# Optimization experiments

Hardware: AMD Instinct MI355X
Metric: run time of the kernel (lower is better)

The kernel has to match this reference:

```python
import jax, jax.numpy as jnp
import numpy as np
from jax import lax

B, S, H, T = 64, 512, 768, 9


def setup_inputs() -> dict:
    key = jax.random.key(0)
    ks = jax.random.split(key, 7)
    hidden = jax.random.normal(ks[0], (B, S, H), dtype=jnp.float32)
    W = jax.random.normal(ks[1], (H, T), dtype=jnp.float32) * 0.02
    b = jax.random.normal(ks[2], (T,), dtype=jnp.float32) * 0.02
    start_trans = jax.random.normal(ks[3], (T,), dtype=jnp.float32) * 0.1
    end_trans = jax.random.normal(ks[4], (T,), dtype=jnp.float32) * 0.1
    trans = jax.random.normal(ks[5], (T, T), dtype=jnp.float32) * 0.1
    labels = jax.random.randint(ks[6], (B, S), 0, T, dtype=jnp.int64)
    return {"hidden": hidden, "W": W, "b": b, "start_trans": start_trans,
            "end_trans": end_trans, "trans": trans, "labels": labels}


def _crf_nll(emissions, labels, start_trans, end_trans, trans):
    # emissions: [B,S,T], labels: [B,S] int. mask = labels > -1 (torchcrf semantics).
    maskf = (labels > -1).astype(emissions.dtype)          # [B,S]
    tags = jnp.maximum(labels, 0)                          # safe indexing

    # ---- numerator: score of the gold path ----
    tags0 = tags[:, 0]                                     # [B]
    num0 = start_trans[tags0] + jnp.take_along_axis(emissions[:, 0], tags0[:, None], axis=1)[:, 0]

    em_t = jnp.swapaxes(emissions[:, 1:], 0, 1)            # [S-1,B,T]
    tg_t = jnp.swapaxes(tags[:, 1:], 0, 1)                 # [S-1,B]
    mk_t = jnp.swapaxes(maskf[:, 1:], 0, 1)                # [S-1,B]

    def num_step(carry, xs):
        score, prev = carry
        em, tg, mk = xs
        step = trans[prev, tg] + jnp.take_along_axis(em, tg[:, None], axis=1)[:, 0]
        score = score + step * mk
        prev = jnp.where(mk > 0, tg, prev)
        return (score, prev), None

    (num, last_tags), _ = lax.scan(num_step, (num0, tags0), (em_t, tg_t, mk_t))
    num = num + end_trans[last_tags]                       # [B]

    # ---- denominator: log-partition via forward algorithm (log-semiring scan) ----
    alpha0 = start_trans[None, :] + emissions[:, 0]        # [B,T]

    def den_step(alpha, xs):
        em, mk = xs
        new = jax.nn.logsumexp(alpha[:, :, None] + trans[None, :, :], axis=1) + em  # [B,T]
        alpha = jnp.where(mk[:, None] > 0, new, alpha)
        return alpha, None

    alpha, _ = lax.scan(den_step, alpha0, (em_t, mk_t))
    den = jax.nn.logsumexp(alpha + end_trans[None, :], axis=1)  # [B]

    # model returns -crf(...) with reduction='mean'  =>  mean NLL
    return jnp.mean(den - num)


def reference(hidden, W, b, start_trans, end_trans, trans, labels):
    # token-classification head: [B,S,H] @ [H,T] -> emissions [B,S,T]
    emissions = jnp.einsum('bsh,ht->bst', hidden, W) + b
    return _crf_nll(emissions, labels, start_trans, end_trans, trans)
```

## Files before the change

### kernel.cpp

```cpp
#include <hip/hip_runtime.h>

constexpr int Bn = 64, Sn = 512, Hn = 768, Tn = 9;
constexpr int EMS = 12;
constexpr int CHUNKS = 32, CLEN = 16;
constexpr int WPAD = 776;

__device__ __forceinline__ float lse9(const float* e) {
    float m01 = fmaxf(e[0], e[1]), m23 = fmaxf(e[2], e[3]);
    float m45 = fmaxf(e[4], e[5]), m67 = fmaxf(e[6], e[7]);
    float m = fmaxf(fmaxf(fmaxf(m01, m23), fmaxf(m45, m67)), e[8]);
    float s = 0.f;
#pragma unroll
    for (int k = 0; k < 9; ++k) s += __expf(e[k] - m);
    return m + __logf(s);
}

__global__ __launch_bounds__(256, 1) void emis_kernel(
        const float* __restrict__ hidden, const float* __restrict__ W,
        const float* __restrict__ bias, float* __restrict__ em) {
    __shared__ float Wt[Tn * WPAD];
    const int tid = threadIdx.x;
    const int lane = tid & 63;

    for (int f = tid; f < Hn * Tn; f += 256) {
        int h = f / 9, t = f - 9 * h;
        Wt[t * WPAD + h] = W[f];
    }
    const float myb = (lane < 9) ? bias[lane] : 0.f;
    __syncthreads();

    float4 wq[27];
#pragma unroll
    for (int t = 0; t < 9; ++t)
#pragma unroll
        for (int k = 0; k < 3; ++k)
            wq[t * 3 + k] = *reinterpret_cast<const float4*>(
                &Wt[t * WPAD + 4 * lane + 256 * k]);

    const int wid = blockIdx.x * 4 + (tid >> 6);
    const int nw  = gridDim.x * 4;
    const int nrows = Bn * Sn;

    int row = wid;
    const float4* hp = reinterpret_cast<const float4*>(hidden + (size_t)row * Hn);
    float4 p0 = hp[lane], p1 = hp[lane + 64], p2 = hp[lane + 128];

    for (; row < nrows; ) {
        const int nxt = row + nw;
        float4 c0 = p0, c1 = p1, c2 = p2;
        if (nxt < nrows) {
            const float4* hq = reinterpret_cast<const float4*>(hidden + (size_t)nxt * Hn);
            p0 = hq[lane]; p1 = hq[lane + 64]; p2 = hq[lane + 128];
        }
        const float hv[12] = {c0.x, c0.y, c0.z, c0.w, c1.x, c1.y, c1.z, c1.w,
                              c2.x, c2.y, c2.z, c2.w};
        float acc[9];
#pragma unroll
        for (int t = 0; t < 9; ++t) acc[t] = 0.f;
#pragma unroll
        for (int k = 0; k < 3; ++k)
#pragma unroll
            for (int c = 0; c < 4; ++c)
#pragma unroll
                for (int t = 0; t < 9; ++t)
                    acc[t] = fmaf(hv[4 * k + c], ((const float*)&wq[t * 3 + k])[c], acc[t]);
#pragma unroll
        for (int m = 1; m < 64; m <<= 1)
#pragma unroll
            for (int t = 0; t < 9; ++t) acc[t] += __shfl_xor(acc[t], m, 64);
        float v = acc[0];
#pragma unroll
        for (int t = 1; t < 9; ++t) v = (lane == t) ? acc[t] : v;
        if (lane < 9) em[(size_t)row * EMS + lane] = v + myb;
        row = nxt;
    }
}

__global__ __launch_bounds__(128) void chunk_kernel(
        const float* __restrict__ em, const float* __restrict__ trans,
        const int* __restrict__ labels, float* __restrict__ Mws) {
    const int b = blockIdx.x / CHUNKS;
    const int c = blockIdx.x % CHUNKS;
    const int tid = threadIdx.x;
    const bool act = tid < 81;
    const int i = tid / 9, j = tid % 9;
    __shared__ float Mbuf[2][9][12];
    __shared__ float emch[CLEN][EMS];
    __shared__ int   labch[CLEN];
    const int s0 = c * CLEN;
    const float* emb = em + ((size_t)b * Sn + s0) * EMS;
    for (int idx = tid; idx < CLEN * EMS; idx += 128)
        (&emch[0][0])[idx] = emb[idx];
    if (tid < CLEN) labch[tid] = labels[b * Sn + s0 + tid];
    float tc[9], row[9];
    float nv = (i == j) ? 0.f : -1e30f;
    if (act) {
#pragma unroll
        for (int k = 0; k < 9; ++k) tc[k] = trans[k * 9 + j];
#pragma unroll
        for (int k = 0; k < 9; ++k) row[k] = (k == i) ? 0.f : -1e30f;
    }
    __syncthreads();
    const int sbeg = (c == 0) ? 1 : 0;
    for (int sl = sbeg; sl < CLEN; ++sl) {
        if (act) {
            float e[9];
#pragma unroll
            for (int k = 0; k < 9; ++k) e[k] = row[k] + tc[k];
            float cand = lse9(e) + emch[sl][j];
            if (labch[sl] > -1) nv = cand;
            Mbuf[sl & 1][i][j] = nv;
        }
        __syncthreads();
        if (act) {
#pragma unroll
            for (int k = 0; k < 9; ++k) row[k] = Mbuf[sl & 1][i][k];
        }
    }
    if (act) Mws[(size_t)(b * CHUNKS + c) * 81 + tid] = nv;
}

__global__ __launch_bounds__(128) void final_kernel(
        const float* __restrict__ em, const float* __restrict__ Mws,
        const float* __restrict__ start, const float* __restrict__ endt,
        const float* __restrict__ trans, const int* __restrict__ labels,
        float* __restrict__ out) {
    const int b = blockIdx.x, tid = threadIdx.x;
    __shared__ float Ml[CHUNKS][9][12];
    __shared__ float red[128];
    for (int idx = tid; idx < CHUNKS * 81; idx += 128) {
        int c = idx / 81, r = idx % 81;
        Ml[c][r / 9][r % 9] = Mws[(size_t)(b * CHUNKS + c) * 81 + r];
    }
    const int* lb = labels + b * Sn;
    float np = 0.f;
    for (int s = tid; s < Sn; s += 128) {
        if (s >= 1) {
            int l = lb[s];
            if (l > -1) {
                int tp = lb[s - 1]; tp = tp > -1 ? tp : 0;
                np += trans[tp * 9 + l] + em[((size_t)b * Sn + s) * EMS + l];
            }
        }
    }
    red[tid] = np;
    __syncthreads();
    for (int off = 64; off > 0; off >>= 1) {
        if (tid < off) red[tid] += red[tid + off];
        __syncthreads();
    }
    if (tid < 9) {
        const int j = tid;
        float alpha[9];
#pragma unroll
        for (int k = 0; k < 9; ++k)
            alpha[k] = start[k] + em[(size_t)b * Sn * EMS + k];
        for (int c = 0; c < CHUNKS; ++c) {
            float e[9];
#pragma unroll
            for (int k = 0; k < 9; ++k) e[k] = alpha[k] + Ml[c][k][j];
            float nv = lse9(e);
#pragma unroll
            for (int k = 0; k < 9; ++k) alpha[k] = __shfl(nv, k, 64);
        }
        if (j == 0) {
            float e[9];
#pragma unroll
            for (int k = 0; k < 9; ++k) e[k] = alpha[k] + endt[k];
            float den = lse9(e);
            int t0 = lb[0] > -1 ? lb[0] : 0;
            float num = red[0] + start[t0] + em[(size_t)b * Sn * EMS + t0];
            int lt = lb[Sn - 1] > -1 ? lb[Sn - 1] : 0;
            num += endt[lt];
            atomicAdd(out, (den - num) * (1.0f / Bn));
        }
    }
}

extern "C" void kernel_launch(void* const* d_in, const int* in_sizes, int n_in,
                              void* d_out, int out_size, void* d_ws, size_t ws_size,
                              hipStream_t stream) {
    const float* hidden = (const float*)d_in[0];
    const float* W      = (const float*)d_in[1];
    const float* bias   = (const float*)d_in[2];
    const float* start  = (const float*)d_in[3];
    const float* endt   = (const float*)d_in[4];
    const float* trans  = (const float*)d_in[5];
    const int*   labels = (const int*)d_in[6];
    float* out = (float*)d_out;

    float* em  = (float*)d_ws;
    float* Mws = em + (size_t)Bn * Sn * EMS;

    hipMemsetAsync(d_out, 0, sizeof(float), stream);
    emis_kernel<<<1024, 256, 0, stream>>>(hidden, W, bias, em);
    chunk_kernel<<<Bn * CHUNKS, 128, 0, stream>>>(em, trans, labels, Mws);
    final_kernel<<<Bn, 128, 0, stream>>>(em, Mws, start, endt, trans, labels, out);
}
```

Baseline: 195.4 us.

## Compute emission projection with bf16 MFMA tiles instead of scalar FMA reductions

The emission GEMV is replaced by a matrix-core path. Each wavefront computes a 16-row by 16-column tile with mfma_f32_16x16x32_bf16, and the W columns are padded from 9 to 16. Hidden values and weights are converted to bf16 in registers, which removes the 9-way cross-lane shuffle reduction and the row-strided loop. The grid is halved so each wave handles exactly 16 rows, and occupancy is raised to 2 blocks. Each lane's loads are strided (16 rows per wave, 32-byte segments), and the reduced precision may shift the final loss beyond tolerance.

```diff
diff --git a/kernel.cpp b/kernel.cpp
--- a/kernel.cpp
+++ b/kernel.cpp
@@ -1,9 +1,18 @@
 #include <hip/hip_runtime.h>
+#include <hip/hip_bf16.h>
 
 constexpr int Bn = 64, Sn = 512, Hn = 768, Tn = 9;
 constexpr int EMS = 12;
 constexpr int CHUNKS = 32, CLEN = 16;
 constexpr int WPAD = 776;
+
+typedef __attribute__((ext_vector_type(8))) short bf16x8;
+typedef __attribute__((ext_vector_type(4))) float f32x4;
+
+__device__ __forceinline__ short f2bf(float x) {
+    __hip_bfloat16 h = __float2bfloat16(x);
+    return *reinterpret_cast<short*>(&h);
+}
 
 __device__ __forceinline__ float lse9(const float* e) {
     float m01 = fmaxf(e[0], e[1]), m23 = fmaxf(e[2], e[3]);
@@ -15,64 +24,50 @@
     return m + __logf(s);
 }
 
-__global__ __launch_bounds__(256, 1) void emis_kernel(
+__global__ __launch_bounds__(256, 2) void emis_kernel(
         const float* __restrict__ hidden, const float* __restrict__ W,
         const float* __restrict__ bias, float* __restrict__ em) {
     __shared__ float Wt[Tn * WPAD];
-    const int tid = threadIdx.x;
-    const int lane = tid & 63;
-
+    const int tid = threadIdx.x, lane = tid & 63;
     for (int f = tid; f < Hn * Tn; f += 256) {
         int h = f / 9, t = f - 9 * h;
         Wt[t * WPAD + h] = W[f];
     }
-    const float myb = (lane < 9) ? bias[lane] : 0.f;
     __syncthreads();
 
-    float4 wq[27];
+    const int c16 = lane & 15, hi = lane >> 4;
+    const bool on = c16 < Tn;
+    bf16x8 bfrag[24];
 #pragma unroll
-    for (int t = 0; t < 9; ++t)
+    for (int m = 0; m < 24; ++m) {
+        bf16x8 bf;
 #pragma unroll
-        for (int k = 0; k < 3; ++k)
-            wq[t * 3 + k] = *reinterpret_cast<const float4*>(
-                &Wt[t * WPAD + 4 * lane + 256 * k]);
+        for (int e = 0; e < 8; ++e) {
+            float w = on ? Wt[c16 * WPAD + 32 * m + hi * 8 + e] : 0.f;
+            bf[e] = f2bf(w);
+        }
+        bfrag[m] = bf;
+    }
+    const float bcol = on ? bias[c16] : 0.f;
 
-    const int wid = blockIdx.x * 4 + (tid >> 6);
-    const int nw  = gridDim.x * 4;
-    const int nrows = Bn * Sn;
+    const int wid  = blockIdx.x * 4 + (tid >> 6);
+    const int row0 = wid * 16;
+    const float* abase = hidden + (size_t)(row0 + c16) * Hn + hi * 8;
 
-    int row = wid;
-    const float4* hp = reinterpret_cast<const float4*>(hidden + (size_t)row * Hn);
-    float4 p0 = hp[lane], p1 = hp[lane + 64], p2 = hp[lane + 128];
-
-    for (; row < nrows; ) {
-        const int nxt = row + nw;
-        float4 c0 = p0, c1 = p1, c2 = p2;
-        if (nxt < nrows) {
-            const float4* hq = reinterpret_cast<const float4*>(hidden + (size_t)nxt * Hn);
-            p0 = hq[lane]; p1 = hq[lane + 64]; p2 = hq[lane + 128];
-        }
-        const float hv[12] = {c0.x, c0.y, c0.z, c0.w, c1.x, c1.y, c1.z, c1.w,
-                              c2.x, c2.y, c2.z, c2.w};
-        float acc[9];
+    f32x4 acc = {0.f, 0.f, 0.f, 0.f};
 #pragma unroll
-        for (int t = 0; t < 9; ++t) acc[t] = 0.f;
+    for (int m = 0; m < 24; ++m) {
+        float4 u0 = *reinterpret_cast<const float4*>(abase + 32 * m);
+        float4 u1 = *reinterpret_cast<const float4*>(abase + 32 * m + 4);
+        bf16x8 af;
+        af[0] = f2bf(u0.x); af[1] = f2bf(u0.y); af[2] = f2bf(u0.z); af[3] = f2bf(u0.w);
+        af[4] = f2bf(u1.x); af[5] = f2bf(u1.y); af[6] = f2bf(u1.z); af[7] = f2bf(u1.w);
+        acc = __builtin_amdgcn_mfma_f32_16x16x32_bf16(af, bfrag[m], acc, 0, 0, 0);
+    }
+    if (on) {
+        float* o = em + (size_t)(row0 + hi * 4) * EMS + c16;
 #pragma unroll
-        for (int k = 0; k < 3; ++k)
-#pragma unroll
-            for (int c = 0; c < 4; ++c)
-#pragma unroll
-                for (int t = 0; t < 9; ++t)
-                    acc[t] = fmaf(hv[4 * k + c], ((const float*)&wq[t * 3 + k])[c], acc[t]);
-#pragma unroll
-        for (int m = 1; m < 64; m <<= 1)
-#pragma unroll
-            for (int t = 0; t < 9; ++t) acc[t] += __shfl_xor(acc[t], m, 64);
-        float v = acc[0];
-#pragma unroll
-        for (int t = 1; t < 9; ++t) v = (lane == t) ? acc[t] : v;
-        if (lane < 9) em[(size_t)row * EMS + lane] = v + myb;
-        row = nxt;
+        for (int i = 0; i < 4; ++i) o[(size_t)i * EMS] = acc[i] + bcol;
     }
 }
 
@@ -193,7 +188,7 @@
     float* Mws = em + (size_t)Bn * Sn * EMS;
 
     hipMemsetAsync(d_out, 0, sizeof(float), stream);
-    emis_kernel<<<1024, 256, 0, stream>>>(hidden, W, bias, em);
+    emis_kernel<<<512, 256, 0, stream>>>(hidden, W, bias, em);
     chunk_kernel<<<Bn * CHUNKS, 128, 0, stream>>>(em, trans, labels, Mws);
     final_kernel<<<Bn, 128, 0, stream>>>(em, Mws, start, endt, trans, labels, out);
 }
```

After: 201.4 us. 1.03x slower.
